# Performance work log

Measured on AMD Instinct MI355X. Metric: run time of the kernel, lower is better.

The kernel has to match this reference:

```python
import jax, jax.numpy as jnp
import numpy as np

N = 200000
F_IN = 165
H = 128
E = 3200000


def gcn_conv(x, edge_index, W, b):
    # x: [N, Fin], edge_index: [2, E], W: [Fin, Fout], b: [Fout]
    n = x.shape[0]
    h = x @ W  # linear transform first (PyG GCNConv)
    # add self loops
    loops = jnp.arange(n, dtype=edge_index.dtype)
    src = jnp.concatenate([edge_index[0], loops])
    dst = jnp.concatenate([edge_index[1], loops])
    # symmetric normalization: deg computed on dst (in-degree incl. self loops)
    deg = jax.ops.segment_sum(jnp.ones_like(dst, dtype=h.dtype), dst, num_segments=n)
    dinv = jnp.where(deg > 0, jax.lax.rsqrt(deg), 0.0)
    norm = dinv[src] * dinv[dst]  # [E+N]
    msgs = h[src] * norm[:, None]  # gather + scale
    out = jax.ops.segment_sum(msgs, dst, num_segments=n)  # scatter-add
    return out + b


def setup_inputs() -> dict:
    key = jax.random.key(0)
    k = jax.random.split(key, 8)
    x = jax.random.normal(k[0], (N, F_IN), dtype=jnp.float32)
    edge_index = jax.random.randint(k[1], (2, E), 0, N, dtype=jnp.int64)
    s1 = 1.0 / np.sqrt(F_IN)
    s2 = 1.0 / np.sqrt(H)
    W1 = jax.random.uniform(k[2], (F_IN, H), jnp.float32, -s1, s1)
    b1 = jnp.zeros((H,), jnp.float32)
    W2 = jax.random.uniform(k[3], (H, H), jnp.float32, -s2, s2)
    b2 = jnp.zeros((H,), jnp.float32)
    Wl = jax.random.uniform(k[4], (H, 2), jnp.float32, -s2, s2)
    bl = jax.random.uniform(k[5], (2,), jnp.float32, -s2, s2)
    return {"x": x, "edge_index": edge_index, "W1": W1, "b1": b1,
            "W2": W2, "b2": b2, "Wl": Wl, "bl": bl}


def reference(x, edge_index, W1, b1, W2, b2, Wl, bl):
    h = gcn_conv(x, edge_index, W1, b1)
    h = jax.nn.relu(h)
    # dropout p=0.3 is identity in eval mode
    h = gcn_conv(h, edge_index, W2, b2)
    h = jax.nn.relu(h)
    return h @ Wl + bl  # [N, 2]
```

## Files before the change

### kernel.cpp

```cpp
#include <hip/hip_runtime.h>
#include <hip/hip_bf16.h>

#define FIN 165
#define HID 128
#define NPB 256
#define MAXNB 784
#define CAP 4608
#define EPB 4096

typedef __attribute__((ext_vector_type(8))) short short8;
typedef __attribute__((ext_vector_type(4))) float float4v;

__device__ inline unsigned bf16rne(float v) {
    unsigned u = __float_as_uint(v);
    return (u + 0x7fffu + ((u >> 16) & 1u)) >> 16;
}

__device__ inline void bf16split(float v, short& h, short& l) {
    unsigned u = __float_as_uint(v);
    unsigned r = u + 0x7fffu + ((u >> 16) & 1u);
    h = (short)(r >> 16);
    float hf = __uint_as_float(((unsigned)(unsigned short)h) << 16);
    float lf = v - hf;
    unsigned u2 = __float_as_uint(lf);
    unsigned r2 = u2 + 0x7fffu + ((u2 >> 16) & 1u);
    l = (short)(r2 >> 16);
}

__global__ __launch_bounds__(256) void bucket_scatter(const int* __restrict__ src,
                                                      const int* __restrict__ dst,
                                                      int* __restrict__ gcur,
                                                      int2* __restrict__ bucketed,
                                                      int E, int n, int NB) {
    __shared__ int hist[MAXNB];
    __shared__ int base[MAXNB];
    __shared__ int lcur[MAXNB];
    int tid = threadIdx.x;
    long e0 = (long)blockIdx.x * EPB;
    for (int b = tid; b < NB; b += 256) { hist[b] = 0; lcur[b] = 0; }
    __syncthreads();
#pragma unroll
    for (int i = 0; i < EPB / 256; ++i) {
        long e = e0 + i * 256 + tid;
        if (e < E) {
            int d = dst[e], s = src[e];
            if ((unsigned)d < (unsigned)n && (unsigned)s < (unsigned)n)
                atomicAdd(&hist[d >> 8], 1);
        }
    }
    __syncthreads();
    for (int b = tid; b < NB; b += 256) {
        int h = hist[b];
        base[b] = h ? atomicAdd(&gcur[b * 16], h) : 0;
    }
    __syncthreads();
#pragma unroll
    for (int i = 0; i < EPB / 256; ++i) {
        long e = e0 + i * 256 + tid;
        if (e < E) {
            int d = dst[e], s = src[e];
            if ((unsigned)d < (unsigned)n && (unsigned)s < (unsigned)n) {
                int bk = d >> 8;
                int idx = base[bk] + atomicAdd(&lcur[bk], 1);
                if ((unsigned)idx < (unsigned)CAP)
                    bucketed[(size_t)bk * CAP + idx] = make_int2(s, d);
            }
        }
    }
}

__global__ __launch_bounds__(256) void bucket_scan(const int* __restrict__ gcur,
                                                   int* __restrict__ bb, int NB,
                                                   int* __restrict__ rowptr, int n) {
    __shared__ int sm[MAXNB];
    for (int b = threadIdx.x; b < NB; b += 256) sm[b] = gcur[b * 16];
    __syncthreads();
    if (threadIdx.x == 0) {
        int run = 0;
        for (int b = 0; b < NB; ++b) { int c = sm[b]; sm[b] = run; run += c; }
        bb[NB] = run;
        rowptr[n] = run;
    }
    __syncthreads();
    for (int b = threadIdx.x; b < NB; b += 256) bb[b] = sm[b];
}

__global__ __launch_bounds__(256) void build_csr(const int2* __restrict__ bucketed,
                                                 const int* __restrict__ bb,
                                                 float* __restrict__ dinv,
                                                 int* __restrict__ rowptr,
                                                 int* __restrict__ col, int n) {
    __shared__ int deg[NPB];
    __shared__ int scn[NPB];
    __shared__ int cur[NPB];
    int b = blockIdx.x, tid = threadIdx.x;
    int nb0 = b * NPB;
    int ebase = bb[b], cnt = bb[b + 1] - bb[b];
    deg[tid] = 0;
    __syncthreads();
    const int2* ep = bucketed + (size_t)b * CAP;
    for (int i = tid; i < cnt; i += 256) {
        int2 e = ep[i];
        atomicAdd(&deg[e.y - nb0], 1);
    }
    __syncthreads();
    int d = deg[tid];
    scn[tid] = d;
    __syncthreads();
    for (int off = 1; off < 256; off <<= 1) {
        int v = (tid >= off) ? scn[tid - off] : 0;
        __syncthreads();
        scn[tid] += v;
        __syncthreads();
    }
    int excl = scn[tid] - d;
    int node = nb0 + tid;
    if (node < n) {
        dinv[node] = rsqrtf((float)(d + 1));
        rowptr[node] = ebase + excl;
    }
    cur[tid] = excl;
    __syncthreads();
    for (int i = tid; i < cnt; i += 256) {
        int2 e = ep[i];
        int p = atomicAdd(&cur[e.y - nb0], 1);
        col[ebase + p] = e.x;
    }
}

__global__ __launch_bounds__(256) void wswz(const float* __restrict__ W,
                                            short8* __restrict__ out, int K, int k32) {
    int idx = blockIdx.x * 256 + threadIdx.x;
    int tot = k32 * 8 * 64;
    if (idx >= tot) return;
    int lane = idx & 63;
    int ct = (idx >> 6) & 7;
    int ks = idx >> 9;
    int col = ct * 16 + (lane & 15);
    int kb = ks * 32 + (lane >> 4) * 8;
    short8 hi, lo;
#pragma unroll
    for (int j = 0; j < 8; ++j) {
        int k = kb + j;
        float v = (k < K) ? W[k * HID + col] : 0.f;
        short h, l;
        bf16split(v, h, l);
        hi[j] = h; lo[j] = l;
    }
    out[idx] = hi;
    out[tot + idx] = lo;
}

__global__ __launch_bounds__(256) void gemm_mfma(const float* __restrict__ X,
                                                 const short8* __restrict__ Wsw,
                                                 const float* __restrict__ dinv,
                                                 unsigned* __restrict__ H2,
                                                 int n, int K, int kfull, int k32) {
    int wave = threadIdx.x >> 6, lane = threadIdx.x & 63;
    int r0 = blockIdx.x * 64 + wave * 16;
    int m = lane & 15, kph = lane >> 4;
    int row = r0 + m;
    const float* xrow = X + (size_t)row * K + kph * 8;
    const short8* Whi = Wsw;
    const short8* Wlo = Wsw + (size_t)k32 * 8 * 64;

    float4v acc[8];
#pragma unroll
    for (int ct = 0; ct < 8; ++ct) acc[ct] = (float4v){0.f, 0.f, 0.f, 0.f};

    for (int ks = 0; ks < kfull; ++ks) {
        float xv[8];
#pragma unroll
        for (int j = 0; j < 8; ++j) xv[j] = xrow[ks * 32 + j];
        short8 ah, al;
#pragma unroll
        for (int j = 0; j < 8; ++j) {
            short h, l; bf16split(xv[j], h, l);
            ah[j] = h; al[j] = l;
        }
#pragma unroll
        for (int ct = 0; ct < 8; ++ct) {
            short8 bh = Whi[(ks * 8 + ct) * 64 + lane];
            short8 bl = Wlo[(ks * 8 + ct) * 64 + lane];
            acc[ct] = __builtin_amdgcn_mfma_f32_16x16x32_bf16(ah, bh, acc[ct], 0, 0, 0);
            acc[ct] = __builtin_amdgcn_mfma_f32_16x16x32_bf16(al, bh, acc[ct], 0, 0, 0);
            acc[ct] = __builtin_amdgcn_mfma_f32_16x16x32_bf16(ah, bl, acc[ct], 0, 0, 0);
        }
    }
    if (kfull < k32) {
        int ks = kfull;
        int kb = ks * 32 + kph * 8;
        float xv[8];
#pragma unroll
        for (int j = 0; j < 8; ++j) xv[j] = (kb + j < K) ? xrow[ks * 32 + j] : 0.f;
        short8 ah, al;
#pragma unroll
        for (int j = 0; j < 8; ++j) {
            short h, l; bf16split(xv[j], h, l);
            ah[j] = h; al[j] = l;
        }
#pragma unroll
        for (int ct = 0; ct < 8; ++ct) {
            short8 bh = Whi[(ks * 8 + ct) * 64 + lane];
            short8 bl = Wlo[(ks * 8 + ct) * 64 + lane];
            acc[ct] = __builtin_amdgcn_mfma_f32_16x16x32_bf16(ah, bh, acc[ct], 0, 0, 0);
            acc[ct] = __builtin_amdgcn_mfma_f32_16x16x32_bf16(al, bh, acc[ct], 0, 0, 0);
            acc[ct] = __builtin_amdgcn_mfma_f32_16x16x32_bf16(ah, bl, acc[ct], 0, 0, 0);
        }
    }
    int ccol = lane & 15, crow = (lane >> 4) * 4;
    bool evenl = (ccol & 1) == 0;
#pragma unroll
    for (int r = 0; r < 4; ++r) {
        int gr = r0 + crow + r;
        float s = dinv[gr];
#pragma unroll
        for (int ct = 0; ct < 8; ++ct) {
            float v = acc[ct][r] * s;
            float p = __shfl_xor(v, 1);
            if (evenl) {
                unsigned u = bf16rne(v) | (bf16rne(p) << 16);
                H2[(size_t)gr * 64 + ct * 8 + (ccol >> 1)] = u;
            }
        }
    }
}

__device__ inline void bf2_unpack(unsigned u, float& f0, float& f1) {
    f0 = __uint_as_float(u << 16);
    f1 = __uint_as_float(u & 0xffff0000u);
}

__global__ __launch_bounds__(256) void agg_relu(const unsigned* __restrict__ HS2,
                                                const int* __restrict__ rowptr,
                                                const int* __restrict__ col,
                                                const float* __restrict__ dinv,
                                                const float* __restrict__ bias,
                                                float* __restrict__ Y, int n) {
    int lane = threadIdx.x & 63;
    int node = __builtin_amdgcn_readfirstlane(blockIdx.x * 4 + (threadIdx.x >> 6));
    if (node >= n) return;
    int start = __builtin_amdgcn_readfirstlane(rowptr[node]);
    int end   = __builtin_amdgcn_readfirstlane(rowptr[node + 1]);
    float2 acc;
    {
        float f0, f1;
        bf2_unpack(HS2[(size_t)node * 64 + lane], f0, f1);
        acc.x = f0; acc.y = f1;
    }
    int j = start;
    for (; j + 16 <= end; j += 16) {
        unsigned uv[16];
#pragma unroll
        for (int q = 0; q < 16; ++q) {
            int c = col[j + q];
            uv[q] = HS2[(size_t)c * 64 + lane];
        }
#pragma unroll
        for (int q = 0; q < 16; ++q) {
            float f0, f1; bf2_unpack(uv[q], f0, f1);
            acc.x += f0; acc.y += f1;
        }
    }
    while (j < end) {
        unsigned uv[8];
#pragma unroll
        for (int q = 0; q < 8; ++q) {
            int jq = j + q;
            int c = (jq < end) ? col[jq] : node;
            uv[q] = HS2[(size_t)c * 64 + lane];
        }
#pragma unroll
        for (int q = 0; q < 8; ++q) {
            unsigned u = (j + q < end) ? uv[q] : 0u;
            float f0, f1; bf2_unpack(u, f0, f1);
            acc.x += f0; acc.y += f1;
        }
        j += 8;
    }
    float s = dinv[node];
    float2 b = *(const float2*)&bias[2 * lane];
    float2 o;
    o.x = fmaxf(acc.x * s + b.x, 0.f);
    o.y = fmaxf(acc.y * s + b.y, 0.f);
    *(float2*)&Y[(long)node * HID + 2 * lane] = o;
}

__global__ __launch_bounds__(256) void agg_relu_head(const unsigned* __restrict__ HS2,
                                                     const int* __restrict__ rowptr,
                                                     const int* __restrict__ col,
                                                     const float* __restrict__ dinv,
                                                     const float* __restrict__ bias,
                                                     const float* __restrict__ Wl,
                                                     const float* __restrict__ bl,
                                                     float* __restrict__ out, int n) {
    int lane = threadIdx.x & 63;
    int node = __builtin_amdgcn_readfirstlane(blockIdx.x * 4 + (threadIdx.x >> 6));
    if (node >= n) return;
    int start = __builtin_amdgcn_readfirstlane(rowptr[node]);
    int end   = __builtin_amdgcn_readfirstlane(rowptr[node + 1]);
    float2 acc;
    {
        float f0, f1;
        bf2_unpack(HS2[(size_t)node * 64 + lane], f0, f1);
        acc.x = f0; acc.y = f1;
    }
    int j = start;
    for (; j + 16 <= end; j += 16) {
        unsigned uv[16];
#pragma unroll
        for (int q = 0; q < 16; ++q) {
            int c = col[j + q];
            uv[q] = HS2[(size_t)c * 64 + lane];
        }
#pragma unroll
        for (int q = 0; q < 16; ++q) {
            float f0, f1; bf2_unpack(uv[q], f0, f1);
            acc.x += f0; acc.y += f1;
        }
    }
    while (j < end) {
        unsigned uv[8];
#pragma unroll
        for (int q = 0; q < 8; ++q) {
            int jq = j + q;
            int c = (jq < end) ? col[jq] : node;
            uv[q] = HS2[(size_t)c * 64 + lane];
        }
#pragma unroll
        for (int q = 0; q < 8; ++q) {
            unsigned u = (j + q < end) ? uv[q] : 0u;
            float f0, f1; bf2_unpack(u, f0, f1);
            acc.x += f0; acc.y += f1;
        }
        j += 8;
    }
    float s = dinv[node];
    float2 b = *(const float2*)&bias[2 * lane];
    float vx = fmaxf(acc.x * s + b.x, 0.f);
    float vy = fmaxf(acc.y * s + b.y, 0.f);
    float4 wl = *(const float4*)&Wl[4 * lane];
    float a0 = vx * wl.x + vy * wl.z;
    float a1 = vx * wl.y + vy * wl.w;
#pragma unroll
    for (int off = 32; off > 0; off >>= 1) {
        a0 += __shfl_xor(a0, off);
        a1 += __shfl_xor(a1, off);
    }
    if (lane == 0) {
        out[node * 2 + 0] = a0 + bl[0];
        out[node * 2 + 1] = a1 + bl[1];
    }
}

extern "C" void kernel_launch(void* const* d_in, const int* in_sizes, int n_in,
                              void* d_out, int out_size, void* d_ws, size_t ws_size,
                              hipStream_t stream) {
    const float* x  = (const float*)d_in[0];
    const int*   ei = (const int*)d_in[1];
    const float* W1 = (const float*)d_in[2];
    const float* b1 = (const float*)d_in[3];
    const float* W2 = (const float*)d_in[4];
    const float* b2 = (const float*)d_in[5];
    const float* Wl = (const float*)d_in[6];
    const float* bl = (const float*)d_in[7];
    float* out = (float*)d_out;

    int n = in_sizes[0] / FIN;
    int E = in_sizes[1] / 2;
    int NB = (n + NPB - 1) / NPB;
    const int* srcp = ei;
    const int* dstp = ei + E;

    char* w = (char*)d_ws;
    auto alloc = [&](size_t bytes) {
        char* p = w;
        w += (bytes + 255) & ~(size_t)255;
        return (void*)p;
    };
    int*      gcur    = (int*)     alloc((size_t)NB * 16 * 4);
    int*      bb      = (int*)     alloc(((size_t)NB + 1) * 4);
    int*      rowptr  = (int*)     alloc(((size_t)n + 1) * 4);
    float*    dinv    = (float*)   alloc((size_t)n * 4);
    int*      colv    = (int*)     alloc((size_t)E * 4);
    unsigned* hbuf    = (unsigned*)alloc((size_t)n * 64 * 4);
    float*    ybuf    = (float*)   alloc((size_t)n * HID * 4);
    const int K32_1 = (FIN + 31) / 32;
    const int K32_2 = HID / 32;
    short8*   w1sw    = (short8*)  alloc((size_t)2 * K32_1 * 8 * 64 * 16);
    short8*   w2sw    = (short8*)  alloc((size_t)2 * K32_2 * 8 * 64 * 16);
    int2*     bucketed = (int2*)ybuf;

    hipMemsetAsync(gcur, 0, (size_t)NB * 16 * 4, stream);

    wswz<<<(K32_1 * 8 * 64 + 255) / 256, 256, 0, stream>>>(W1, w1sw, FIN, K32_1);
    wswz<<<(K32_2 * 8 * 64 + 255) / 256, 256, 0, stream>>>(W2, w2sw, HID, K32_2);

    bucket_scatter<<<(E + EPB - 1) / EPB, 256, 0, stream>>>(srcp, dstp, gcur,
                                                            bucketed, E, n, NB);
    bucket_scan<<<1, 256, 0, stream>>>(gcur, bb, NB, rowptr, n);
    build_csr<<<NB, 256, 0, stream>>>(bucketed, bb, dinv, rowptr, colv, n);

    gemm_mfma<<<n / 64, 256, 0, stream>>>(x, w1sw, dinv, hbuf, n, FIN, FIN / 32, K32_1);
    agg_relu<<<(n + 3) / 4, 256, 0, stream>>>(hbuf, rowptr, colv, dinv, b1, ybuf, n);

    gemm_mfma<<<n / 64, 256, 0, stream>>>(ybuf, w2sw, dinv, hbuf, n, HID, HID / 32, K32_2);

    agg_relu_head<<<(n + 3) / 4, 256, 0, stream>>>(hbuf, rowptr, colv, dinv, b2,
                                                   Wl, bl, out, n);
}
```

Baseline: 703.8 us.

## Pack bucketed edges into 32-bit words, cache edge loads, parallelize bucket scan

```diff
diff --git a/kernel.cpp b/kernel.cpp
--- a/kernel.cpp
+++ b/kernel.cpp
@@ -6,7 +6,7 @@
 #define NPB 256
 #define MAXNB 784
 #define CAP 4608
-#define EPB 4096
+#define EPB 2048
 
 typedef __attribute__((ext_vector_type(8))) short short8;
 typedef __attribute__((ext_vector_type(4))) float float4v;
@@ -30,7 +30,7 @@
 __global__ __launch_bounds__(256) void bucket_scatter(const int* __restrict__ src,
                                                       const int* __restrict__ dst,
                                                       int* __restrict__ gcur,
-                                                      int2* __restrict__ bucketed,
+                                                      unsigned* __restrict__ bucketed,
                                                       int E, int n, int NB) {
     __shared__ int hist[MAXNB];
     __shared__ int base[MAXNB];
@@ -39,14 +39,14 @@
     long e0 = (long)blockIdx.x * EPB;
     for (int b = tid; b < NB; b += 256) { hist[b] = 0; lcur[b] = 0; }
     __syncthreads();
+    int sv[EPB / 256], dv[EPB / 256];
 #pragma unroll
     for (int i = 0; i < EPB / 256; ++i) {
         long e = e0 + i * 256 + tid;
-        if (e < E) {
-            int d = dst[e], s = src[e];
-            if ((unsigned)d < (unsigned)n && (unsigned)s < (unsigned)n)
-                atomicAdd(&hist[d >> 8], 1);
-        }
+        sv[i] = (e < E) ? src[e] : -1;
+        dv[i] = (e < E) ? dst[e] : -1;
+        if ((unsigned)dv[i] < (unsigned)n && (unsigned)sv[i] < (unsigned)n)
+            atomicAdd(&hist[dv[i] >> 8], 1);
     }
     __syncthreads();
     for (int b = tid; b < NB; b += 256) {
@@ -56,15 +56,13 @@
     __syncthreads();
 #pragma unroll
     for (int i = 0; i < EPB / 256; ++i) {
-        long e = e0 + i * 256 + tid;
-        if (e < E) {
-            int d = dst[e], s = src[e];
-            if ((unsigned)d < (unsigned)n && (unsigned)s < (unsigned)n) {
-                int bk = d >> 8;
-                int idx = base[bk] + atomicAdd(&lcur[bk], 1);
-                if ((unsigned)idx < (unsigned)CAP)
-                    bucketed[(size_t)bk * CAP + idx] = make_int2(s, d);
-            }
+        int d = dv[i], s = sv[i];
+        if ((unsigned)d < (unsigned)n && (unsigned)s < (unsigned)n) {
+            int bk = d >> 8;
+            int idx = base[bk] + atomicAdd(&lcur[bk], 1);
+            if ((unsigned)idx < (unsigned)CAP)
+                bucketed[(size_t)bk * CAP + idx] =
+                    (unsigned)s | ((unsigned)(d & 255) << 18);
         }
     }
 }
@@ -72,20 +70,35 @@
 __global__ __launch_bounds__(256) void bucket_scan(const int* __restrict__ gcur,
                                                    int* __restrict__ bb, int NB,
                                                    int* __restrict__ rowptr, int n) {
-    __shared__ int sm[MAXNB];
-    for (int b = threadIdx.x; b < NB; b += 256) sm[b] = gcur[b * 16];
-    __syncthreads();
-    if (threadIdx.x == 0) {
-        int run = 0;
-        for (int b = 0; b < NB; ++b) { int c = sm[b]; sm[b] = run; run += c; }
-        bb[NB] = run;
-        rowptr[n] = run;
-    }
-    __syncthreads();
-    for (int b = threadIdx.x; b < NB; b += 256) bb[b] = sm[b];
-}
-
-__global__ __launch_bounds__(256) void build_csr(const int2* __restrict__ bucketed,
+    __shared__ int part[256];
+    int t = threadIdx.x;
+    int v[4];
+    int s = 0;
+#pragma unroll
+    for (int i = 0; i < 4; ++i) {
+        int b = t * 4 + i;
+        v[i] = (b < NB) ? gcur[b * 16] : 0;
+        s += v[i];
+    }
+    part[t] = s;
+    __syncthreads();
+    for (int off = 1; off < 256; off <<= 1) {
+        int x = (t >= off) ? part[t - off] : 0;
+        __syncthreads();
+        part[t] += x;
+        __syncthreads();
+    }
+    int run = part[t] - s;
+#pragma unroll
+    for (int i = 0; i < 4; ++i) {
+        int b = t * 4 + i;
+        if (b < NB) bb[b] = run;
+        run += v[i];
+    }
+    if (t == 255) { bb[NB] = run; rowptr[n] = run; }
+}
+
+__global__ __launch_bounds__(256) void build_csr(const unsigned* __restrict__ bucketed,
                                                  const int* __restrict__ bb,
                                                  float* __restrict__ dinv,
                                                  int* __restrict__ rowptr,
@@ -98,10 +111,10 @@
     int ebase = bb[b], cnt = bb[b + 1] - bb[b];
     deg[tid] = 0;
     __syncthreads();
-    const int2* ep = bucketed + (size_t)b * CAP;
+    const unsigned* ep = bucketed + (size_t)b * CAP;
     for (int i = tid; i < cnt; i += 256) {
-        int2 e = ep[i];
-        atomicAdd(&deg[e.y - nb0], 1);
+        unsigned v = ep[i];
+        atomicAdd(&deg[(v >> 18) & 255], 1);
     }
     __syncthreads();
     int d = deg[tid];
@@ -122,9 +135,9 @@
     cur[tid] = excl;
     __syncthreads();
     for (int i = tid; i < cnt; i += 256) {
-        int2 e = ep[i];
-        int p = atomicAdd(&cur[e.y - nb0], 1);
-        col[ebase + p] = e.x;
+        unsigned v = ep[i];
+        int p = atomicAdd(&cur[(v >> 18) & 255], 1);
+        col[ebase + p] = (int)(v & 0x3FFFFu);
     }
 }
 
@@ -389,7 +402,7 @@
     const int K32_2 = HID / 32;
     short8*   w1sw    = (short8*)  alloc((size_t)2 * K32_1 * 8 * 64 * 16);
     short8*   w2sw    = (short8*)  alloc((size_t)2 * K32_2 * 8 * 64 * 16);
-    int2*     bucketed = (int2*)ybuf;
+    unsigned* bucketed = (unsigned*)ybuf;
 
     hipMemsetAsync(gcur, 0, (size_t)NB * 16 * 4, stream);
 
```

After: 701.5 us. About the same (-0.3%).
